# Kernel optimization log

Hardware: AMD Instinct MI355X
Metric: run time of the kernel (lower is better)

The kernel has to match this reference:

```python
import jax, jax.numpy as jnp
import numpy as np

D_IN = 1024
D_OUT = 1024
NUM_HEADS = 16
HEAD_DIM = D_OUT // NUM_HEADS


def setup_inputs() -> dict:
    key = jax.random.key(0)
    ks = jax.random.split(key, 6)
    s = 0.02
    x = jax.random.normal(ks[0], (1, 4096, D_IN), dtype=jnp.float32)
    W_q = jax.random.normal(ks[1], (D_IN, D_OUT), dtype=jnp.float32) * s
    W_k = jax.random.normal(ks[2], (D_IN, D_OUT), dtype=jnp.float32) * s
    W_v = jax.random.normal(ks[3], (D_IN, D_OUT), dtype=jnp.float32) * s
    W_o = jax.random.normal(ks[4], (D_OUT, D_OUT), dtype=jnp.float32) * s
    b_o = jnp.zeros((D_OUT,), dtype=jnp.float32)
    return {"x": x, "W_q": W_q, "W_k": W_k, "W_v": W_v, "W_o": W_o, "b_o": b_o}


def reference(x, W_q, W_k, W_v, W_o, b_o):
    b, n, _ = x.shape
    # project and split heads: [b, h, n, d]
    def split_heads(t):
        return t.reshape(b, n, NUM_HEADS, HEAD_DIM).transpose(0, 2, 1, 3)
    q = split_heads(x @ W_q)
    k = split_heads(x @ W_k)
    v = split_heads(x @ W_v)
    scale = 1.0 / jnp.sqrt(jnp.float32(HEAD_DIM))
    scores = jnp.einsum('bhqd,bhkd->bhqk', q, k) * scale  # [b,h,n,n]
    causal = jnp.tril(jnp.ones((n, n), dtype=bool))
    scores = jnp.where(causal, scores, -jnp.inf)
    weights = jax.nn.softmax(scores, axis=-1)
    # dropout rate is 0.0 -> identity
    ctx = jnp.einsum('bhqk,bhkd->bhqd', weights, v)
    ctx = ctx.transpose(0, 2, 1, 3).reshape(b, n, D_OUT)
    return ctx @ W_o + b_o
```

## Files before the change

kernel.cpp:

```cpp
#include <hip/hip_runtime.h>
#include <hip/hip_bf16.h>

typedef __hip_bfloat16 bf16;
typedef __attribute__((ext_vector_type(8))) short short8;
typedef __attribute__((ext_vector_type(4))) float floatx4;

#define SEQ 4096
#define DIM 1024
#define NH 16
#define HD 64

#if defined(__has_builtin)
#if __has_builtin(__builtin_amdgcn_exp2f)
#define EXP2(x) __builtin_amdgcn_exp2f(x)
#endif
#endif
#ifndef EXP2
#define EXP2(x) exp2f(x)
#endif

__device__ __forceinline__ short f2s(float f) { bf16 t = __float2bfloat16(f); return *(short*)&t; }

__device__ __forceinline__ void gload16(const void* g, void* l) {
    __builtin_amdgcn_global_load_lds(
        (const __attribute__((address_space(1))) void*)g,
        (__attribute__((address_space(3))) void*)l, 16, 0, 0);
}

__device__ __forceinline__ void barrier_lgkm() {
    asm volatile("s_waitcnt lgkmcnt(0)" ::: "memory");
    __builtin_amdgcn_s_barrier();
}

__device__ __forceinline__ short8 cvt8(float4 a, float4 b) {
    short8 s;
    s[0] = f2s(a.x); s[1] = f2s(a.y); s[2] = f2s(a.z); s[3] = f2s(a.w);
    s[4] = f2s(b.x); s[5] = f2s(b.y); s[6] = f2s(b.z); s[7] = f2s(b.w);
    return s;
}

__global__ __launch_bounds__(256) void transpose_cast_kernel(
    const float* __restrict__ W0, const float* __restrict__ W1,
    const float* __restrict__ W2, const float* __restrict__ W3,
    bf16* __restrict__ Wt_all)
{
    const float* W = blockIdx.z == 0 ? W0 : blockIdx.z == 1 ? W1
                   : blockIdx.z == 2 ? W2 : W3;
    bf16* Wt = Wt_all + (size_t)blockIdx.z * DIM * DIM;

    __shared__ float tile[32][33];
    const int n0 = blockIdx.x * 32, k0 = blockIdx.y * 32;
    const int tr = threadIdx.x >> 5;
    const int tc = threadIdx.x & 31;
#pragma unroll
    for (int i = 0; i < 32; i += 8)
        tile[tr + i][tc] = W[(size_t)(k0 + tr + i) * DIM + n0 + tc];
    __syncthreads();
#pragma unroll
    for (int i = 0; i < 32; i += 8)
        Wt[(size_t)(n0 + tr + i) * DIM + k0 + tc] = __float2bfloat16(tile[tc][tr + i]);
}

#define QBM 128
#define QBN 128
#define QBK 64

__global__ __launch_bounds__(256) void qkv_gemm_kernel(
    const float* __restrict__ A, const bf16* __restrict__ Wt,
    bf16* __restrict__ Qb, bf16* __restrict__ Kb, bf16* __restrict__ Vb)
{
    const int z = blockIdx.z;
    const bf16* Bt = Wt + (size_t)z * DIM * DIM;
    bf16* C = z == 0 ? Qb : (z == 1 ? Kb : Vb);
    const float osc = (z == 0) ? 0.18033688f : 1.0f;

    __shared__ alignas(16) float Af[QBM][QBK];
    __shared__ alignas(16) short Bs[QBN][QBK];

    const int tid  = threadIdx.x;
    const int wave = tid >> 6, lane = tid & 63;
    const int l15  = lane & 15, quad = lane >> 4;
    const int wm = (wave & 1) * 64;
    const int wn = (wave >> 1) * 64;
    const int bm = blockIdx.y * QBM;
    const int bn = blockIdx.x * QBN;

    const int arow = tid >> 4;
    const int agch = (tid & 15) ^ (arow & 15);
    const float* gA = A + (size_t)(bm + arow) * DIM + agch * 4;
    char* ldsA = (char*)&Af[0][0] + wave * 1024;

    const int brow = tid >> 3;
    const int bgch = (tid & 7) ^ (brow & 7);
    const bf16* gB = Bt + (size_t)(bn + brow) * DIM + bgch * 8;
    char* ldsB = (char*)&Bs[0][0] + wave * 1024;

    floatx4 acc[4][4] = {};

    for (int k0 = 0; k0 < DIM; k0 += QBK) {
        __syncthreads();
#pragma unroll
        for (int c = 0; c < 8; ++c)
            gload16(gA + (size_t)c * 16 * DIM + k0, ldsA + c * 4096);
#pragma unroll
        for (int c = 0; c < 4; ++c)
            gload16(gB + (size_t)c * 32 * DIM + k0, ldsB + c * 4096);
        __syncthreads();

#pragma unroll
        for (int c2 = 0; c2 < 2; ++c2) {
            const int g0 = c2 * 8 + quad * 2;
            const int cb = (c2 * 4 + quad) ^ (l15 & 7);
            short8 afr[4], bfr[4];
#pragma unroll
            for (int i = 0; i < 4; ++i) {
                const int ra = wm + i * 16 + l15;
                float4 f0 = *(const float4*)&Af[ra][(g0 ^ l15) * 4];
                float4 f1 = *(const float4*)&Af[ra][((g0 + 1) ^ l15) * 4];
                afr[i] = cvt8(f0, f1);
                bfr[i] = *(const short8*)&Bs[wn + i * 16 + l15][cb * 8];
            }
#pragma unroll
            for (int mi = 0; mi < 4; ++mi)
#pragma unroll
                for (int ni = 0; ni < 4; ++ni)
                    acc[mi][ni] = __builtin_amdgcn_mfma_f32_16x16x32_bf16(
                        afr[mi], bfr[ni], acc[mi][ni], 0, 0, 0);
        }
    }

#pragma unroll
    for (int mi = 0; mi < 4; ++mi)
#pragma unroll
        for (int r = 0; r < 4; ++r) {
            const int row = bm + wm + mi * 16 + quad * 4 + r;
#pragma unroll
            for (int ni = 0; ni < 4; ++ni) {
                const int col = bn + wn + ni * 16 + l15;
                C[(size_t)row * DIM + col] = __float2bfloat16(acc[mi][ni][r] * osc);
            }
        }
}

__global__ __launch_bounds__(256) void out_gemm_kernel(
    const bf16* __restrict__ A, const bf16* __restrict__ Bt,
    const float* __restrict__ bias, float* __restrict__ C)
{
    __shared__ alignas(16) short Asl[128][64];
    __shared__ alignas(16) short Bsl[64][64];

    const int tid  = threadIdx.x;
    const int wave = tid >> 6, lane = tid & 63;
    const int l15  = lane & 15, quad = lane >> 4;
    const int wm = (wave & 1) * 64;
    const int wn = (wave >> 1) * 32;
    const int bm = blockIdx.y * 128;
    const int bn = blockIdx.x * 64;

    const int srow   = tid >> 3;
    const int gchunk = (tid & 7) ^ (srow & 7);
    const bf16* gA = A  + (size_t)(bm + srow) * DIM + gchunk * 8;
    const bf16* gB = Bt + (size_t)(bn + srow) * DIM + gchunk * 8;
    char* ldsA = (char*)&Asl[0][0] + wave * 1024;
    char* ldsB = (char*)&Bsl[0][0] + wave * 1024;

    floatx4 acc[4][2] = {};

    for (int k0 = 0; k0 < DIM; k0 += 64) {
        __syncthreads();
#pragma unroll
        for (int c = 0; c < 4; ++c)
            gload16(gA + (size_t)c * 32 * DIM + k0, ldsA + c * 4096);
#pragma unroll
        for (int c = 0; c < 2; ++c)
            gload16(gB + (size_t)c * 32 * DIM + k0, ldsB + c * 4096);
        __syncthreads();

#pragma unroll
        for (int c2 = 0; c2 < 2; ++c2) {
            const int cb = (c2 * 4 + quad) ^ (l15 & 7);
            short8 afr[4], bfr[2];
#pragma unroll
            for (int i = 0; i < 4; ++i)
                afr[i] = *(const short8*)&Asl[wm + i * 16 + l15][cb * 8];
#pragma unroll
            for (int i = 0; i < 2; ++i)
                bfr[i] = *(const short8*)&Bsl[wn + i * 16 + l15][cb * 8];
#pragma unroll
            for (int mi = 0; mi < 4; ++mi)
#pragma unroll
                for (int ni = 0; ni < 2; ++ni)
                    acc[mi][ni] = __builtin_amdgcn_mfma_f32_16x16x32_bf16(
                        afr[mi], bfr[ni], acc[mi][ni], 0, 0, 0);
        }
    }

#pragma unroll
    for (int mi = 0; mi < 4; ++mi)
#pragma unroll
        for (int r = 0; r < 4; ++r) {
            const int row = bm + wm + mi * 16 + quad * 4 + r;
#pragma unroll
            for (int ni = 0; ni < 2; ++ni) {
                const int col = bn + wn + ni * 16 + l15;
                C[(size_t)row * DIM + col] = acc[mi][ni][r] + bias[col];
            }
        }
}

#define QT 128
#define KT 64
#define LDT 72

__global__ __launch_bounds__(256) void flash_attn_kernel(
    const bf16* __restrict__ Q, const bf16* __restrict__ K,
    const bf16* __restrict__ V, bf16* ctx)
{
    const int lin  = blockIdx.y * 32 + blockIdx.x;
    const int half = lin >> 8, idx = lin & 255;
    const int qj   = half ? (idx & 31) : 31 - (idx & 31);
    const int h    = (idx >> 5) + 8 * half;
    const int q0   = qj * QT;
    const int nkt  = 2 * qj + 2;

    const int tid  = threadIdx.x;
    const int wave = tid >> 6;
    const int lane = tid & 63;
    const int l15  = lane & 15;
    const int quad = lane >> 4;

    __shared__ alignas(16) short Ks[2][KT][LDT];
    __shared__ alignas(16) short Vt[2][HD][LDT];

    short8 qfrag[2][2];
#pragma unroll
    for (int s = 0; s < 2; ++s) {
        const bf16* qp = Q + (size_t)(q0 + wave * 32 + s * 16 + l15) * DIM
                       + h * HD + quad * 8;
#pragma unroll
        for (int c = 0; c < 2; ++c)
            qfrag[s][c] = *(const short8*)(qp + c * 32);
    }

    const int kr = tid >> 2, kc = (tid & 3) * 16;
    const int vr = (tid & 31) * 2, vd = (tid >> 5) * 8;
    const int vslot = ((vr >> 5) & 1) * 32 + ((vr >> 2) & 3) * 8
                    + ((vr >> 4) & 1) * 4  + ((vr >> 1) & 1) * 2;

    short8 kreg0, kreg1, vreg0, vreg1;
    {
        const short8* kp  = (const short8*)(K + (size_t)kr * DIM + h * HD + kc);
        kreg0 = kp[0]; kreg1 = kp[1];
        const short8* vp0 = (const short8*)(V + (size_t)vr * DIM + h * HD + vd);
        const short8* vp1 = (const short8*)(V + (size_t)(vr + 1) * DIM + h * HD + vd);
        vreg0 = vp0[0]; vreg1 = vp1[0];
    }
    *(short8*)&Ks[0][kr][kc]     = kreg0;
    *(short8*)&Ks[0][kr][kc + 8] = kreg1;
#pragma unroll
    for (int i = 0; i < 8; ++i) {
        unsigned int pv = (unsigned int)(unsigned short)vreg0[i]
                        | ((unsigned int)(unsigned short)vreg1[i] << 16);
        *(unsigned int*)&Vt[0][vd + i][vslot] = pv;
    }
    {
        const size_t nb = (size_t)KT;
        const short8* kp  = (const short8*)(K + (nb + kr) * DIM + h * HD + kc);
        kreg0 = kp[0]; kreg1 = kp[1];
        const short8* vp0 = (const short8*)(V + (nb + vr) * DIM + h * HD + vd);
        const short8* vp1 = (const short8*)(V + (nb + vr + 1) * DIM + h * HD + vd);
        vreg0 = vp0[0]; vreg1 = vp1[0];
    }

    barrier_lgkm();

    short8 onesf;
#pragma unroll
    for (int i = 0; i < 8; ++i) onesf[i] = (short)0x3F80;

    floatx4 o_acc[2][4] = {};
    floatx4 lacc[2] = {};

    for (int kt = 0; kt < nkt; ++kt) {
        const int b = kt & 1;

        floatx4 sT[2][4] = {};
#pragma unroll
        for (int n = 0; n < 4; ++n)
#pragma unroll
            for (int c = 0; c < 2; ++c) {
                short8 kf = *(const short8*)&Ks[b][n * 16 + l15][c * 32 + quad * 8];
#pragma unroll
                for (int s = 0; s < 2; ++s)
                    sT[s][n] = __builtin_amdgcn_mfma_f32_16x16x32_bf16(
                        kf, qfrag[s][c], sT[s][n], 0, 0, 0);
            }

        if (kt + 1 < nkt) {
            *(short8*)&Ks[b ^ 1][kr][kc]     = kreg0;
            *(short8*)&Ks[b ^ 1][kr][kc + 8] = kreg1;
#pragma unroll
            for (int i = 0; i < 8; ++i) {
                unsigned int pv = (unsigned int)(unsigned short)vreg0[i]
                                | ((unsigned int)(unsigned short)vreg1[i] << 16);
                *(unsigned int*)&Vt[b ^ 1][vd + i][vslot] = pv;
            }
            if (kt + 2 < nkt) {
                const size_t nb = (size_t)(kt + 2) * KT;
                const short8* kp  = (const short8*)(K + (nb + kr) * DIM + h * HD + kc);
                kreg0 = kp[0]; kreg1 = kp[1];
                const short8* vp0 = (const short8*)(V + (nb + vr) * DIM + h * HD + vd);
                const short8* vp1 = (const short8*)(V + (nb + vr + 1) * DIM + h * HD + vd);
                vreg0 = vp0[0]; vreg1 = vp1[0];
            }
        }

        short8 pfrag[2][2];
        const int kbase = kt * KT;
        if (kt >= nkt - 2) {
#pragma unroll
            for (int s = 0; s < 2; ++s) {
                const int qrow = q0 + wave * 32 + s * 16 + l15;
                float p[4][4];
#pragma unroll
                for (int n = 0; n < 4; ++n) {
                    const int key0 = kbase + n * 16 + quad * 4;
#pragma unroll
                    for (int r = 0; r < 4; ++r)
                        p[n][r] = (key0 + r <= qrow) ? EXP2(sT[s][n][r]) : 0.f;
                }
#pragma unroll
                for (int c = 0; c < 2; ++c) {
                    short8 f;
#pragma unroll
                    for (int j = 0; j < 8; ++j)
                        f[j] = f2s(p[c * 2 + (j >> 2)][j & 3]);
                    pfrag[s][c] = f;
                }
            }
        } else {
#pragma unroll
            for (int s = 0; s < 2; ++s)
#pragma unroll
                for (int c = 0; c < 2; ++c) {
                    short8 f;
#pragma unroll
                    for (int j = 0; j < 8; ++j)
                        f[j] = f2s(EXP2(sT[s][c * 2 + (j >> 2)][j & 3]));
                    pfrag[s][c] = f;
                }
        }

#pragma unroll
        for (int n = 0; n < 4; ++n)
#pragma unroll
            for (int c = 0; c < 2; ++c) {
                short8 vf = *(const short8*)&Vt[b][n * 16 + l15][c * 32 + quad * 8];
#pragma unroll
                for (int s = 0; s < 2; ++s)
                    o_acc[s][n] = __builtin_amdgcn_mfma_f32_16x16x32_bf16(
                        pfrag[s][c], vf, o_acc[s][n], 0, 0, 0);
            }
#pragma unroll
        for (int s = 0; s < 2; ++s) {
            lacc[s] = __builtin_amdgcn_mfma_f32_16x16x32_bf16(pfrag[s][0], onesf, lacc[s], 0, 0, 0);
            lacc[s] = __builtin_amdgcn_mfma_f32_16x16x32_bf16(pfrag[s][1], onesf, lacc[s], 0, 0, 0);
        }

        barrier_lgkm();
    }

#pragma unroll
    for (int s = 0; s < 2; ++s)
#pragma unroll
        for (int r = 0; r < 4; ++r) {
            const float inv = 1.0f / lacc[s][r];
            const int row = q0 + wave * 32 + s * 16 + quad * 4 + r;
#pragma unroll
            for (int n = 0; n < 4; ++n)
                ctx[(size_t)row * DIM + h * HD + n * 16 + l15] =
                    __float2bfloat16(o_acc[s][n][r] * inv);
        }
}

extern "C" void kernel_launch(void* const* d_in, const int* in_sizes, int n_in,
                              void* d_out, int out_size, void* d_ws, size_t ws_size,
                              hipStream_t stream)
{
    const float* x  = (const float*)d_in[0];
    const float* Wq = (const float*)d_in[1];
    const float* Wk = (const float*)d_in[2];
    const float* Wv = (const float*)d_in[3];
    const float* Wo = (const float*)d_in[4];
    const float* bo = (const float*)d_in[5];
    float* out = (float*)d_out;

    bf16* Wt_all = (bf16*)d_ws;
    bf16* Qb     = Wt_all + (size_t)4 * DIM * DIM;
    bf16* V      = (bf16*)d_out;
    bf16* Kb     = V + (size_t)SEQ * DIM;
    bf16* ctx    = Qb;
    const bf16* Wot = Wt_all + (size_t)3 * DIM * DIM;

    transpose_cast_kernel<<<dim3(32, 32, 4), 256, 0, stream>>>(Wq, Wk, Wv, Wo, Wt_all);

    qkv_gemm_kernel<<<dim3(DIM / QBN, SEQ / QBM, 3), 256, 0, stream>>>(
        x, Wt_all, Qb, Kb, V);

    flash_attn_kernel<<<dim3(32, NH), 256, 0, stream>>>(Qb, Kb, V, ctx);

    out_gemm_kernel<<<dim3(DIM / 64, SEQ / 128), 256, 0, stream>>>(
        ctx, Wot, bo, out);
}
```

Before: 195.7 us.

## Use 8 waves per attention block with 16 query rows each

The flash attention kernel now launches 512 threads (8 waves) per 128-row query tile, and each wave handles 16 query rows instead of 32. K staging is spread across all threads and V transpose staging uses the first 256 threads. The aim is more waves per CU to hide latency, and fewer registers per wave from halving the accumulators. The cost is that each K/V fragment read from LDS is reused by one MFMA instead of two, which doubles LDS read traffic per unit of work.

```diff
diff --git a/kernel.cpp b/kernel.cpp
--- a/kernel.cpp
+++ b/kernel.cpp
@@ -212,7 +212,7 @@
 #define KT 64
 #define LDT 72
 
-__global__ __launch_bounds__(256) void flash_attn_kernel(
+__global__ __launch_bounds__(512) void flash_attn_kernel(
     const bf16* __restrict__ Q, const bf16* __restrict__ K,
     const bf16* __restrict__ V, bf16* ctx)
 {
@@ -232,44 +232,39 @@
     __shared__ alignas(16) short Ks[2][KT][LDT];
     __shared__ alignas(16) short Vt[2][HD][LDT];
 
-    short8 qfrag[2][2];
-#pragma unroll
-    for (int s = 0; s < 2; ++s) {
-        const bf16* qp = Q + (size_t)(q0 + wave * 32 + s * 16 + l15) * DIM
+    short8 qfrag[2];
+    {
+        const bf16* qp = Q + (size_t)(q0 + wave * 16 + l15) * DIM
                        + h * HD + quad * 8;
-#pragma unroll
-        for (int c = 0; c < 2; ++c)
-            qfrag[s][c] = *(const short8*)(qp + c * 32);
-    }
-
-    const int kr = tid >> 2, kc = (tid & 3) * 16;
-    const int vr = (tid & 31) * 2, vd = (tid >> 5) * 8;
+        qfrag[0] = *(const short8*)(qp);
+        qfrag[1] = *(const short8*)(qp + 32);
+    }
+
+    const int kr = tid >> 3, kc = (tid & 7) * 8;
+    const bool vstager = tid < 256;
+    const int vr = (tid & 31) * 2, vd = ((tid >> 5) & 7) * 8;
     const int vslot = ((vr >> 5) & 1) * 32 + ((vr >> 2) & 3) * 8
                     + ((vr >> 4) & 1) * 4  + ((vr >> 1) & 1) * 2;
 
-    short8 kreg0, kreg1, vreg0, vreg1;
-    {
-        const short8* kp  = (const short8*)(K + (size_t)kr * DIM + h * HD + kc);
-        kreg0 = kp[0]; kreg1 = kp[1];
-        const short8* vp0 = (const short8*)(V + (size_t)vr * DIM + h * HD + vd);
-        const short8* vp1 = (const short8*)(V + (size_t)(vr + 1) * DIM + h * HD + vd);
-        vreg0 = vp0[0]; vreg1 = vp1[0];
-    }
-    *(short8*)&Ks[0][kr][kc]     = kreg0;
-    *(short8*)&Ks[0][kr][kc + 8] = kreg1;
-#pragma unroll
-    for (int i = 0; i < 8; ++i) {
-        unsigned int pv = (unsigned int)(unsigned short)vreg0[i]
-                        | ((unsigned int)(unsigned short)vreg1[i] << 16);
-        *(unsigned int*)&Vt[0][vd + i][vslot] = pv;
-    }
-    {
-        const size_t nb = (size_t)KT;
-        const short8* kp  = (const short8*)(K + (nb + kr) * DIM + h * HD + kc);
-        kreg0 = kp[0]; kreg1 = kp[1];
-        const short8* vp0 = (const short8*)(V + (nb + vr) * DIM + h * HD + vd);
-        const short8* vp1 = (const short8*)(V + (nb + vr + 1) * DIM + h * HD + vd);
-        vreg0 = vp0[0]; vreg1 = vp1[0];
+    short8 kreg, vreg0, vreg1;
+    kreg = *(const short8*)(K + (size_t)kr * DIM + h * HD + kc);
+    if (vstager) {
+        vreg0 = *(const short8*)(V + (size_t)vr * DIM + h * HD + vd);
+        vreg1 = *(const short8*)(V + (size_t)(vr + 1) * DIM + h * HD + vd);
+    }
+    *(short8*)&Ks[0][kr][kc] = kreg;
+    if (vstager) {
+#pragma unroll
+        for (int i = 0; i < 8; ++i) {
+            unsigned int pv = (unsigned int)(unsigned short)vreg0[i]
+                            | ((unsigned int)(unsigned short)vreg1[i] << 16);
+            *(unsigned int*)&Vt[0][vd + i][vslot] = pv;
+        }
+    }
+    kreg = *(const short8*)(K + (size_t)(KT + kr) * DIM + h * HD + kc);
+    if (vstager) {
+        vreg0 = *(const short8*)(V + (size_t)(KT + vr) * DIM + h * HD + vd);
+        vreg1 = *(const short8*)(V + (size_t)(KT + vr + 1) * DIM + h * HD + vd);
     }
 
     barrier_lgkm();
@@ -278,77 +273,71 @@
 #pragma unroll
     for (int i = 0; i < 8; ++i) onesf[i] = (short)0x3F80;
 
-    floatx4 o_acc[2][4] = {};
-    floatx4 lacc[2] = {};
+    floatx4 o_acc[4] = {};
+    floatx4 lacc = {};
 
     for (int kt = 0; kt < nkt; ++kt) {
         const int b = kt & 1;
 
-        floatx4 sT[2][4] = {};
+        floatx4 sT[4] = {};
 #pragma unroll
         for (int n = 0; n < 4; ++n)
 #pragma unroll
             for (int c = 0; c < 2; ++c) {
                 short8 kf = *(const short8*)&Ks[b][n * 16 + l15][c * 32 + quad * 8];
-#pragma unroll
-                for (int s = 0; s < 2; ++s)
-                    sT[s][n] = __builtin_amdgcn_mfma_f32_16x16x32_bf16(
-                        kf, qfrag[s][c], sT[s][n], 0, 0, 0);
+                sT[n] = __builtin_amdgcn_mfma_f32_16x16x32_bf16(
+                    kf, qfrag[c], sT[n], 0, 0, 0);
             }
 
         if (kt + 1 < nkt) {
-            *(short8*)&Ks[b ^ 1][kr][kc]     = kreg0;
-            *(short8*)&Ks[b ^ 1][kr][kc + 8] = kreg1;
-#pragma unroll
-            for (int i = 0; i < 8; ++i) {
-                unsigned int pv = (unsigned int)(unsigned short)vreg0[i]
-                                | ((unsigned int)(unsigned short)vreg1[i] << 16);
-                *(unsigned int*)&Vt[b ^ 1][vd + i][vslot] = pv;
+            *(short8*)&Ks[b ^ 1][kr][kc] = kreg;
+            if (vstager) {
+#pragma unroll
+                for (int i = 0; i < 8; ++i) {
+                    unsigned int pv = (unsigned int)(unsigned short)vreg0[i]
+                                    | ((unsigned int)(unsigned short)vreg1[i] << 16);
+                    *(unsigned int*)&Vt[b ^ 1][vd + i][vslot] = pv;
+                }
             }
             if (kt + 2 < nkt) {
                 const size_t nb = (size_t)(kt + 2) * KT;
-                const short8* kp  = (const short8*)(K + (nb + kr) * DIM + h * HD + kc);
-                kreg0 = kp[0]; kreg1 = kp[1];
-                const short8* vp0 = (const short8*)(V + (nb + vr) * DIM + h * HD + vd);
-                const short8* vp1 = (const short8*)(V + (nb + vr + 1) * DIM + h * HD + vd);
-                vreg0 = vp0[0]; vreg1 = vp1[0];
-            }
-        }
-
-        short8 pfrag[2][2];
+                kreg = *(const short8*)(K + (nb + kr) * DIM + h * HD + kc);
+                if (vstager) {
+                    vreg0 = *(const short8*)(V + (nb + vr) * DIM + h * HD + vd);
+                    vreg1 = *(const short8*)(V + (nb + vr + 1) * DIM + h * HD + vd);
+                }
+            }
+        }
+
+        short8 pfrag[2];
         const int kbase = kt * KT;
         if (kt >= nkt - 2) {
-#pragma unroll
-            for (int s = 0; s < 2; ++s) {
-                const int qrow = q0 + wave * 32 + s * 16 + l15;
-                float p[4][4];
-#pragma unroll
-                for (int n = 0; n < 4; ++n) {
-                    const int key0 = kbase + n * 16 + quad * 4;
-#pragma unroll
-                    for (int r = 0; r < 4; ++r)
-                        p[n][r] = (key0 + r <= qrow) ? EXP2(sT[s][n][r]) : 0.f;
-                }
-#pragma unroll
-                for (int c = 0; c < 2; ++c) {
-                    short8 f;
-#pragma unroll
-                    for (int j = 0; j < 8; ++j)
-                        f[j] = f2s(p[c * 2 + (j >> 2)][j & 3]);
-                    pfrag[s][c] = f;
-                }
+            const int qrow = q0 + wave * 16 + l15;
+            float p[4][4];
+#pragma unroll
+            for (int n = 0; n < 4; ++n) {
+                const int key0 = kbase + n * 16 + quad * 4;
+#pragma unroll
+                for (int r = 0; r < 4; ++r)
+                    p[n][r] = (key0 + r <= qrow) ? EXP2(sT[n][r]) : 0.f;
+            }
+#pragma unroll
+            for (int c = 0; c < 2; ++c) {
+                short8 f;
+#pragma unroll
+                for (int j = 0; j < 8; ++j)
+                    f[j] = f2s(p[c * 2 + (j >> 2)][j & 3]);
+                pfrag[c] = f;
             }
         } else {
 #pragma unroll
-            for (int s = 0; s < 2; ++s)
-#pragma unroll
-                for (int c = 0; c < 2; ++c) {
-                    short8 f;
-#pragma unroll
-                    for (int j = 0; j < 8; ++j)
-                        f[j] = f2s(EXP2(sT[s][c * 2 + (j >> 2)][j & 3]));
-                    pfrag[s][c] = f;
-                }
+            for (int c = 0; c < 2; ++c) {
+                short8 f;
+#pragma unroll
+                for (int j = 0; j < 8; ++j)
+                    f[j] = f2s(EXP2(sT[c * 2 + (j >> 2)][j & 3]));
+                pfrag[c] = f;
+            }
         }
 
 #pragma unroll
@@ -356,31 +345,24 @@
 #pragma unroll
             for (int c = 0; c < 2; ++c) {
                 short8 vf = *(const short8*)&Vt[b][n * 16 + l15][c * 32 + quad * 8];
-#pragma unroll
-                for (int s = 0; s < 2; ++s)
-                    o_acc[s][n] = __builtin_amdgcn_mfma_f32_16x16x32_bf16(
-                        pfrag[s][c], vf, o_acc[s][n], 0, 0, 0);
-            }
-#pragma unroll
-        for (int s = 0; s < 2; ++s) {
-            lacc[s] = __builtin_amdgcn_mfma_f32_16x16x32_bf16(pfrag[s][0], onesf, lacc[s], 0, 0, 0);
-            lacc[s] = __builtin_amdgcn_mfma_f32_16x16x32_bf16(pfrag[s][1], onesf, lacc[s], 0, 0, 0);
-        }
+                o_acc[n] = __builtin_amdgcn_mfma_f32_16x16x32_bf16(
+                    pfrag[c], vf, o_acc[n], 0, 0, 0);
+            }
+        lacc = __builtin_amdgcn_mfma_f32_16x16x32_bf16(pfrag[0], onesf, lacc, 0, 0, 0);
+        lacc = __builtin_amdgcn_mfma_f32_16x16x32_bf16(pfrag[1], onesf, lacc, 0, 0, 0);
 
         barrier_lgkm();
     }
 
 #pragma unroll
-    for (int s = 0; s < 2; ++s)
-#pragma unroll
-        for (int r = 0; r < 4; ++r) {
-            const float inv = 1.0f / lacc[s][r];
-            const int row = q0 + wave * 32 + s * 16 + quad * 4 + r;
-#pragma unroll
-            for (int n = 0; n < 4; ++n)
-                ctx[(size_t)row * DIM + h * HD + n * 16 + l15] =
-                    __float2bfloat16(o_acc[s][n][r] * inv);
-        }
+    for (int r = 0; r < 4; ++r) {
+        const float inv = 1.0f / lacc[r];
+        const int row = q0 + wave * 16 + quad * 4 + r;
+#pragma unroll
+        for (int n = 0; n < 4; ++n)
+            ctx[(size_t)row * DIM + h * HD + n * 16 + l15] =
+                __float2bfloat16(o_acc[n][r] * inv);
+    }
 }
 
 extern "C" void kernel_launch(void* const* d_in, const int* in_sizes, int n_in,
@@ -407,7 +389,7 @@
     qkv_gemm_kernel<<<dim3(DIM / QBN, SEQ / QBM, 3), 256, 0, stream>>>(
         x, Wt_all, Qb, Kb, V);
 
-    flash_attn_kernel<<<dim3(32, NH), 256, 0, stream>>>(Qb, Kb, V, ctx);
+    flash_attn_kernel<<<dim3(32, NH), 512, 0, stream>>>(Qb, Kb, V, ctx);
 
     out_gemm_kernel<<<dim3(DIM / 64, SEQ / 128), 256, 0, stream>>>(
         ctx, Wot, bo, out);
```

After: 190.6 us. 1.03x faster.
